# Optimization experiments

Measured on AMD Instinct MI355X. Metric: run time of the kernel, lower is better.

Reference implementation:

```python
import jax, jax.numpy as jnp
import numpy as np

D_IN = 1024
D_OUT = 1024
CTX_LEN = 2048
BATCH = 4
SEQ = 2048


def setup_inputs() -> dict:
    key = jax.random.key(0)
    kx, kq, kk, kv = jax.random.split(key, 4)
    x = jax.random.normal(kx, (BATCH, SEQ, D_IN), dtype=jnp.float32)
    s = 1.0 / np.sqrt(D_IN)
    # torch nn.Linear weight is (d_out, d_in); store transposed for x @ W
    W_q = jax.random.uniform(kq, (D_IN, D_OUT), dtype=jnp.float32, minval=-s, maxval=s)
    W_k = jax.random.uniform(kk, (D_IN, D_OUT), dtype=jnp.float32, minval=-s, maxval=s)
    W_v = jax.random.uniform(kv, (D_IN, D_OUT), dtype=jnp.float32, minval=-s, maxval=s)
    return {"x": x, "W_q": W_q, "W_k": W_k, "W_v": W_v}


def reference(x, W_q, W_k, W_v):
    b, n, _ = x.shape
    d_out = W_q.shape[1]
    q = x @ W_q            # [b, n, d_out]
    k = x @ W_k
    v = x @ W_v
    scores = jnp.einsum('bqd,bkd->bqk', q, k)  # [b, n, n]
    causal = jnp.triu(jnp.ones((n, n), dtype=bool), k=1)
    scores = jnp.where(causal, -jnp.inf, scores)
    attn = jax.nn.softmax(scores / jnp.sqrt(jnp.float32(d_out)), axis=-1)
    # dropout p=0.0 -> identity
    return jnp.einsum('bqk,bkd->bqd', attn, v)
```

## Files before the change

kernel.cpp:

```cpp
#include <hip/hip_runtime.h>
#include <hip/hip_bf16.h>

#define BATCH 4
#define SEQ   2048
#define DIN   1024
#define DOUT  1024
#define N3    3072
#define MTOT  (BATCH*SEQ)

typedef __hip_bfloat16 bf16;
typedef __attribute__((ext_vector_type(8))) short bf16x8;
typedef __attribute__((ext_vector_type(4))) float f32x4;

#define MFMA(a,b,c) __builtin_amdgcn_mfma_f32_16x16x32_bf16(a,b,c,0,0,0)

union pack4 { bf16 h[4]; uint2 u2; };
union pack8 { bf16 h[8]; bf16x8 v; };

__device__ __forceinline__ void gl16(const bf16* g, bf16* l)
{
    __builtin_amdgcn_global_load_lds(
        (const __attribute__((address_space(1))) void*)g,
        (__attribute__((address_space(3))) void*)l, 16, 0, 0);
}


__global__ __launch_bounds__(256)
void k_cvt_x(const float* __restrict__ x, bf16* __restrict__ xb)
{
    long i = ((long)blockIdx.x * 256 + threadIdx.x) * 4;
    float4 v = *(const float4*)(x + i);
    pack4 o;
    o.h[0] = __float2bfloat16(v.x);
    o.h[1] = __float2bfloat16(v.y);
    o.h[2] = __float2bfloat16(v.z);
    o.h[3] = __float2bfloat16(v.w);
    *(uint2*)(xb + i) = o.u2;
}

__global__ __launch_bounds__(256)
void k_cvt_w(const float* __restrict__ Wq, const float* __restrict__ Wk,
             const float* __restrict__ Wv, bf16* __restrict__ Wt)
{
    __shared__ bf16 t[64][68];
    const int mat = blockIdx.z;
    const float* W = (mat == 0) ? Wq : ((mat == 1) ? Wk : Wv);
    const int k0 = blockIdx.y * 64, n0 = blockIdx.x * 64;
#pragma unroll
    for (int p = 0; p < 4; ++p) {
        int kr = p * 16 + (threadIdx.x >> 4);
        int c4 = (threadIdx.x & 15) * 4;
        float4 v = *(const float4*)&W[(long)(k0 + kr) * DOUT + n0 + c4];
        t[c4 + 0][kr] = __float2bfloat16(v.x);
        t[c4 + 1][kr] = __float2bfloat16(v.y);
        t[c4 + 2][kr] = __float2bfloat16(v.z);
        t[c4 + 3][kr] = __float2bfloat16(v.w);
    }
    __syncthreads();
    bf16* O = Wt + (long)mat * DIN * DOUT;
#pragma unroll
    for (int i = 0; i < 2; ++i) {
        int l = threadIdx.x + i * 256;
        int n = l >> 3, c8 = (l & 7) * 8;
        pack8 o;
#pragma unroll
        for (int j = 0; j < 8; ++j) o.h[j] = t[n][c8 + j];
        *(bf16x8*)&O[(long)(n0 + n) * DIN + k0 + c8] = o.v;
    }
}


__device__ __forceinline__ void gemm_core(
    const bf16* __restrict__ Ab, long lda,
    const bf16* __restrict__ Bb, long ldb,
    int nk, bf16* __restrict__ As, bf16* __restrict__ Bs,
    f32x4 acc[4][4])
{
    const int tid  = threadIdx.x;
    const int lane = tid & 63;
    const int wave = tid >> 6;
    const int wm = (wave >> 1) * 64;
    const int wn = (wave & 1) * 64;
    const int r  = lane & 15;
    const int qd = lane >> 4;

    const int row0 = tid >> 3;
    const int c    = (tid & 7) ^ (row0 & 7);
    const long aoff = (long)row0 * lda + c * 8;
    const long boff = (long)row0 * ldb + c * 8;
    const long astep = 32 * lda, bstep = 32 * ldb;
    bf16* dA = &As[tid * 8];
    bf16* dB = &Bs[tid * 8];

    for (int kk = 0; kk < nk; ++kk) {
        const bf16* A = Ab + kk * 64 + aoff;
        const bf16* B = Bb + kk * 64 + boff;
#pragma unroll
        for (int i = 0; i < 4; ++i) {
            gl16(A + i * astep, dA + i * 2048);
            gl16(B + i * bstep, dB + i * 2048);
        }
        __syncthreads();
#pragma unroll
        for (int ks = 0; ks < 2; ++ks) {
            const int slot = ((ks * 4 + qd) ^ (r & 7)) * 8;
            bf16x8 af[4], bv[4];
#pragma unroll
            for (int mi = 0; mi < 4; ++mi)
                af[mi] = *(const bf16x8*)&As[(wm + mi * 16 + r) * 64 + slot];
#pragma unroll
            for (int ni = 0; ni < 4; ++ni)
                bv[ni] = *(const bf16x8*)&Bs[(wn + ni * 16 + r) * 64 + slot];
#pragma unroll
            for (int mi = 0; mi < 4; ++mi)
#pragma unroll
                for (int ni = 0; ni < 4; ++ni)
                    acc[mi][ni] = MFMA(af[mi], bv[ni], acc[mi][ni]);
        }
        __syncthreads();
    }
}


__global__ __launch_bounds__(256)
void k_gemm_qkv(const bf16* __restrict__ xb, const bf16* __restrict__ Wt,
                bf16* __restrict__ QKV)
{
    __shared__ __align__(16) bf16 As[128 * 64];
    __shared__ __align__(16) bf16 Bs[128 * 64];
    const int m0 = blockIdx.y * 128, n0 = blockIdx.x * 128;
    f32x4 acc[4][4] = {};
    gemm_core(xb + (long)m0 * DIN, DIN, Wt + (long)n0 * DIN, DIN, DIN / 64, As, Bs, acc);

    const int lane = threadIdx.x & 63, wave = threadIdx.x >> 6;
    const int wm = (wave >> 1) * 64, wn = (wave & 1) * 64;
    const int r = lane & 15, qd = lane >> 4;
#pragma unroll
    for (int mi = 0; mi < 4; ++mi)
#pragma unroll
        for (int ni = 0; ni < 4; ++ni)
#pragma unroll
            for (int j = 0; j < 4; ++j) {
                int row = m0 + wm + mi * 16 + qd * 4 + j;
                int col = n0 + wn + ni * 16 + r;
                QKV[(long)row * N3 + col] = __float2bfloat16(acc[mi][ni][j]);
            }
}


__global__ __launch_bounds__(256)
void k_transpose_v(const bf16* __restrict__ QKV, bf16* __restrict__ Vt)
{
    __shared__ __align__(16) bf16 t[64][80];
    const int b = blockIdx.z;
    const int s0 = blockIdx.x * 64, d0 = blockIdx.y * 64;
    const bf16* Vb = QKV + (long)b * SEQ * N3 + 2048;
#pragma unroll
    for (int i = 0; i < 2; ++i) {
        int l = threadIdx.x + i * 256;
        int sl = l >> 3, c8 = (l & 7) * 8;
        *(bf16x8*)&t[sl][c8] = *(const bf16x8*)&Vb[(long)(s0 + sl) * N3 + d0 + c8];
    }
    __syncthreads();
    bf16* Ob = Vt + (long)b * DOUT * SEQ;
#pragma unroll
    for (int i = 0; i < 2; ++i) {
        int l = threadIdx.x + i * 256;
        int dl = l >> 3, s8 = (l & 7) * 8;
        pack8 o;
#pragma unroll
        for (int j = 0; j < 8; ++j) o.h[j] = t[s8 + j][dl];
        *(bf16x8*)&Ob[(long)(d0 + dl) * SEQ + s0 + s8] = o.v;
    }
}


__global__ __launch_bounds__(256)
void k_gemm_scores(const bf16* __restrict__ QKV, bf16* __restrict__ P,
                   float* __restrict__ rowSum)
{
    const int b = blockIdx.z, qt = blockIdx.y, kt = blockIdx.x;
    if (kt > qt) return;
    __shared__ __align__(16) bf16 As[128 * 64];
    __shared__ __align__(16) bf16 Bs[128 * 64];
    const bf16* A  = QKV + (long)b * SEQ * N3;
    const bf16* Bt = A + 1024;
    f32x4 acc[4][4] = {};
    gemm_core(A + (long)qt * 128 * N3, N3, Bt + (long)kt * 128 * N3, N3,
              DIN / 64, As, Bs, acc);

    bf16* Pb = P + (long)b * SEQ * SEQ;
    float* RS = rowSum + b * SEQ;
    const int lane = threadIdx.x & 63, wave = threadIdx.x >> 6;
    const int wm = (wave >> 1) * 64, wn = (wave & 1) * 64;
    const int r = lane & 15, qd = lane >> 4;

    float rp[4][4];
#pragma unroll
    for (int mi = 0; mi < 4; ++mi)
#pragma unroll
        for (int j = 0; j < 4; ++j) rp[mi][j] = 0.f;

#pragma unroll
    for (int mi = 0; mi < 4; ++mi)
#pragma unroll
        for (int ni = 0; ni < 4; ++ni)
#pragma unroll
            for (int j = 0; j < 4; ++j) {
                int row = qt * 128 + wm + mi * 16 + qd * 4 + j;
                int col = kt * 128 + wn + ni * 16 + r;
                float e = (col > row) ? 0.f : __expf(acc[mi][ni][j] * 0.03125f);
                rp[mi][j] += e;
                Pb[(long)row * SEQ + col] = __float2bfloat16(e);
            }
#pragma unroll
    for (int d = 1; d < 16; d <<= 1)
#pragma unroll
        for (int mi = 0; mi < 4; ++mi)
#pragma unroll
            for (int j = 0; j < 4; ++j)
                rp[mi][j] += __shfl_xor(rp[mi][j], d, 64);
    if (r == 0) {
#pragma unroll
        for (int mi = 0; mi < 4; ++mi)
#pragma unroll
            for (int j = 0; j < 4; ++j) {
                int row = qt * 128 + wm + mi * 16 + qd * 4 + j;
                atomicAdd(&RS[row], rp[mi][j]);
            }
    }
}


__global__ __launch_bounds__(256)
void k_gemm_pv(const bf16* __restrict__ P, const bf16* __restrict__ Vt,
               const float* __restrict__ rowSum, float* __restrict__ O)
{
    const int b = blockIdx.z, nt = blockIdx.x;
    const int qt = (SEQ / 128 - 1) - blockIdx.y;
    __shared__ __align__(16) bf16 As[128 * 64];
    __shared__ __align__(16) bf16 Bs[128 * 64];
    const bf16* A  = P + (long)b * SEQ * SEQ + (long)qt * 128 * SEQ;
    const bf16* Bt = Vt + (long)b * DOUT * SEQ;
    const int nk = (qt + 1) * 2;
    f32x4 acc[4][4] = {};
    gemm_core(A, SEQ, Bt + (long)nt * 128 * SEQ, SEQ, nk, As, Bs, acc);

    float* Ob = O + (long)b * SEQ * DOUT;
    const float* RS = rowSum + b * SEQ;
    const int lane = threadIdx.x & 63, wave = threadIdx.x >> 6;
    const int wm = (wave >> 1) * 64, wn = (wave & 1) * 64;
    const int r = lane & 15, qd = lane >> 4;
#pragma unroll
    for (int mi = 0; mi < 4; ++mi)
#pragma unroll
        for (int j = 0; j < 4; ++j) {
            int row = qt * 128 + wm + mi * 16 + qd * 4 + j;
            float inv = 1.0f / RS[row];
#pragma unroll
            for (int ni = 0; ni < 4; ++ni) {
                int col = nt * 128 + wn + ni * 16 + r;
                Ob[(long)row * DOUT + col] = acc[mi][ni][j] * inv;
            }
        }
}


extern "C" void kernel_launch(void* const* d_in, const int* in_sizes, int n_in,
                              void* d_out, int out_size, void* d_ws, size_t ws_size,
                              hipStream_t stream)
{
    const float* x  = (const float*)d_in[0];
    const float* Wq = (const float*)d_in[1];
    const float* Wk = (const float*)d_in[2];
    const float* Wv = (const float*)d_in[3];
    float* out = (float*)d_out;

    char* ws = (char*)d_ws;
    bf16*  xb  = (bf16*)(ws);
    bf16*  Wt  = (bf16*)(ws + 16777216);
    bf16*  QKV = (bf16*)(ws + 23068672);
    bf16*  Vt  = (bf16*)(ws + 73400320);
    bf16*  P   = (bf16*)(ws + 90177536);
    float* RS  = (float*)(ws + 123731968);

    hipMemsetAsync(RS, 0, BATCH * SEQ * sizeof(float), stream);
    k_cvt_x<<<dim3(MTOT * DIN / (256 * 4)), 256, 0, stream>>>(x, xb);
    k_cvt_w<<<dim3(DOUT / 64, DIN / 64, 3), 256, 0, stream>>>(Wq, Wk, Wv, Wt);
    k_gemm_qkv<<<dim3(N3 / 128, MTOT / 128), 256, 0, stream>>>(xb, Wt, QKV);
    k_transpose_v<<<dim3(SEQ / 64, DOUT / 64, BATCH), 256, 0, stream>>>(QKV, Vt);
    k_gemm_scores<<<dim3(SEQ / 128, SEQ / 128, BATCH), 256, 0, stream>>>(QKV, P, RS);
    k_gemm_pv<<<dim3(DOUT / 128, SEQ / 128, BATCH), 256, 0, stream>>>(P, Vt, RS, out);
}
```

Before: 254.1 us.

## Fuse V transpose into QKV GEMM epilogue and merge conversion kernels

The QKV projection epilogue now writes Q/K into a compact 2048-wide buffer and transposes V tiles through shared memory directly into Vt, which removes the separate transpose kernel and its extra read and write of V. The x and weight conversion kernels are merged into one launch, and the scores and PV kernels get a launch-bounds occupancy hint of three blocks. This saves two launches and a round trip of V through memory. In exchange the V epilogue adds shared-memory staging and a barrier, and the occupancy hint may push the compiler to spill registers.

```diff
diff --git a/kernel.cpp b/kernel.cpp
--- a/kernel.cpp
+++ b/kernel.cpp
@@ -26,26 +26,28 @@
 
 
 __global__ __launch_bounds__(256)
-void k_cvt_x(const float* __restrict__ x, bf16* __restrict__ xb)
-{
-    long i = ((long)blockIdx.x * 256 + threadIdx.x) * 4;
-    float4 v = *(const float4*)(x + i);
-    pack4 o;
-    o.h[0] = __float2bfloat16(v.x);
-    o.h[1] = __float2bfloat16(v.y);
-    o.h[2] = __float2bfloat16(v.z);
-    o.h[3] = __float2bfloat16(v.w);
-    *(uint2*)(xb + i) = o.u2;
-}
-
-__global__ __launch_bounds__(256)
-void k_cvt_w(const float* __restrict__ Wq, const float* __restrict__ Wk,
-             const float* __restrict__ Wv, bf16* __restrict__ Wt)
+void k_prep(const float* __restrict__ x, const float* __restrict__ Wq,
+            const float* __restrict__ Wk, const float* __restrict__ Wv,
+            bf16* __restrict__ xb, bf16* __restrict__ Wt)
 {
     __shared__ bf16 t[64][68];
-    const int mat = blockIdx.z;
+    const int bid = blockIdx.x;
+    if (bid < 8192) {
+        long i = ((long)bid * 256 + threadIdx.x) * 4;
+        float4 v = *(const float4*)(x + i);
+        pack4 o;
+        o.h[0] = __float2bfloat16(v.x);
+        o.h[1] = __float2bfloat16(v.y);
+        o.h[2] = __float2bfloat16(v.z);
+        o.h[3] = __float2bfloat16(v.w);
+        *(uint2*)(xb + i) = o.u2;
+        return;
+    }
+    const int idx = bid - 8192;
+    const int mat = idx >> 8;
+    const int rem = idx & 255;
+    const int k0 = (rem >> 4) * 64, n0 = (rem & 15) * 64;
     const float* W = (mat == 0) ? Wq : ((mat == 1) ? Wk : Wv);
-    const int k0 = blockIdx.y * 64, n0 = blockIdx.x * 64;
 #pragma unroll
     for (int p = 0; p < 4; ++p) {
         int kr = p * 16 + (threadIdx.x >> 4);
@@ -124,69 +126,73 @@
 
 __global__ __launch_bounds__(256)
 void k_gemm_qkv(const bf16* __restrict__ xb, const bf16* __restrict__ Wt,
-                bf16* __restrict__ QKV)
-{
-    __shared__ __align__(16) bf16 As[128 * 64];
-    __shared__ __align__(16) bf16 Bs[128 * 64];
+                bf16* __restrict__ QK, bf16* __restrict__ Vt)
+{
+    __shared__ __align__(16) bf16 smem[17408];
+    bf16* As = smem;
+    bf16* Bs = smem + 8192;
     const int m0 = blockIdx.y * 128, n0 = blockIdx.x * 128;
     f32x4 acc[4][4] = {};
     gemm_core(xb + (long)m0 * DIN, DIN, Wt + (long)n0 * DIN, DIN, DIN / 64, As, Bs, acc);
 
-    const int lane = threadIdx.x & 63, wave = threadIdx.x >> 6;
+    const int tid = threadIdx.x;
+    const int lane = tid & 63, wave = tid >> 6;
     const int wm = (wave >> 1) * 64, wn = (wave & 1) * 64;
     const int r = lane & 15, qd = lane >> 4;
-#pragma unroll
-    for (int mi = 0; mi < 4; ++mi)
-#pragma unroll
-        for (int ni = 0; ni < 4; ++ni)
-#pragma unroll
-            for (int j = 0; j < 4; ++j) {
-                int row = m0 + wm + mi * 16 + qd * 4 + j;
-                int col = n0 + wn + ni * 16 + r;
-                QKV[(long)row * N3 + col] = __float2bfloat16(acc[mi][ni][j]);
-            }
-}
-
-
-__global__ __launch_bounds__(256)
-void k_transpose_v(const bf16* __restrict__ QKV, bf16* __restrict__ Vt)
-{
-    __shared__ __align__(16) bf16 t[64][80];
-    const int b = blockIdx.z;
-    const int s0 = blockIdx.x * 64, d0 = blockIdx.y * 64;
-    const bf16* Vb = QKV + (long)b * SEQ * N3 + 2048;
-#pragma unroll
-    for (int i = 0; i < 2; ++i) {
-        int l = threadIdx.x + i * 256;
-        int sl = l >> 3, c8 = (l & 7) * 8;
-        *(bf16x8*)&t[sl][c8] = *(const bf16x8*)&Vb[(long)(s0 + sl) * N3 + d0 + c8];
-    }
-    __syncthreads();
-    bf16* Ob = Vt + (long)b * DOUT * SEQ;
-#pragma unroll
-    for (int i = 0; i < 2; ++i) {
-        int l = threadIdx.x + i * 256;
-        int dl = l >> 3, s8 = (l & 7) * 8;
-        pack8 o;
-#pragma unroll
-        for (int j = 0; j < 8; ++j) o.h[j] = t[s8 + j][dl];
-        *(bf16x8*)&Ob[(long)(d0 + dl) * SEQ + s0 + s8] = o.v;
-    }
-}
-
-
-__global__ __launch_bounds__(256)
-void k_gemm_scores(const bf16* __restrict__ QKV, bf16* __restrict__ P,
+
+    if (n0 < 2048) {
+#pragma unroll
+        for (int mi = 0; mi < 4; ++mi)
+#pragma unroll
+            for (int ni = 0; ni < 4; ++ni)
+#pragma unroll
+                for (int j = 0; j < 4; ++j) {
+                    int row = m0 + wm + mi * 16 + qd * 4 + j;
+                    int col = n0 + wn + ni * 16 + r;
+                    QK[(long)row * 2048 + col] = __float2bfloat16(acc[mi][ni][j]);
+                }
+    } else {
+        const int ld = 136;
+        bf16* T = smem;
+#pragma unroll
+        for (int mi = 0; mi < 4; ++mi)
+#pragma unroll
+            for (int ni = 0; ni < 4; ++ni) {
+                pack4 p;
+#pragma unroll
+                for (int j = 0; j < 4; ++j) p.h[j] = __float2bfloat16(acc[mi][ni][j]);
+                int d_l = wn + ni * 16 + r;
+                int s_l = wm + mi * 16 + qd * 4;
+                *(uint2*)&T[d_l * ld + s_l] = p.u2;
+            }
+        __syncthreads();
+        const int n0v = n0 - 2048;
+        const int bb = m0 >> 11;
+        const int s0 = m0 & 2047;
+        bf16* Ob = Vt + (long)bb * DOUT * SEQ + s0;
+#pragma unroll
+        for (int p = 0; p < 8; ++p) {
+            int l = tid + p * 256;
+            int d = l >> 4, s8 = (l & 15) * 8;
+            bf16x8 vv = *(const bf16x8*)&T[d * ld + s8];
+            *(bf16x8*)&Ob[(long)(n0v + d) * SEQ + s8] = vv;
+        }
+    }
+}
+
+
+__global__ __launch_bounds__(256, 3)
+void k_gemm_scores(const bf16* __restrict__ QK, bf16* __restrict__ P,
                    float* __restrict__ rowSum)
 {
     const int b = blockIdx.z, qt = blockIdx.y, kt = blockIdx.x;
     if (kt > qt) return;
     __shared__ __align__(16) bf16 As[128 * 64];
     __shared__ __align__(16) bf16 Bs[128 * 64];
-    const bf16* A  = QKV + (long)b * SEQ * N3;
+    const bf16* A  = QK + (long)b * SEQ * 2048;
     const bf16* Bt = A + 1024;
     f32x4 acc[4][4] = {};
-    gemm_core(A + (long)qt * 128 * N3, N3, Bt + (long)kt * 128 * N3, N3,
+    gemm_core(A + (long)qt * 128 * 2048, 2048, Bt + (long)kt * 128 * 2048, 2048,
               DIN / 64, As, Bs, acc);
 
     bf16* Pb = P + (long)b * SEQ * SEQ;
@@ -232,7 +238,7 @@
 }
 
 
-__global__ __launch_bounds__(256)
+__global__ __launch_bounds__(256, 3)
 void k_gemm_pv(const bf16* __restrict__ P, const bf16* __restrict__ Vt,
                const float* __restrict__ rowSum, float* __restrict__ O)
 {
@@ -277,18 +283,16 @@
     float* out = (float*)d_out;
 
     char* ws = (char*)d_ws;
-    bf16*  xb  = (bf16*)(ws);
-    bf16*  Wt  = (bf16*)(ws + 16777216);
-    bf16*  QKV = (bf16*)(ws + 23068672);
-    bf16*  Vt  = (bf16*)(ws + 73400320);
-    bf16*  P   = (bf16*)(ws + 90177536);
-    float* RS  = (float*)(ws + 123731968);
+    bf16*  xb = (bf16*)(ws);
+    bf16*  Wt = (bf16*)(ws + 16777216);
+    bf16*  QK = (bf16*)(ws + 23068672);
+    bf16*  Vt = (bf16*)(ws + 56623104);
+    bf16*  P  = (bf16*)(ws + 73400320);
+    float* RS = (float*)(ws + 106954752);
 
     hipMemsetAsync(RS, 0, BATCH * SEQ * sizeof(float), stream);
-    k_cvt_x<<<dim3(MTOT * DIN / (256 * 4)), 256, 0, stream>>>(x, xb);
-    k_cvt_w<<<dim3(DOUT / 64, DIN / 64, 3), 256, 0, stream>>>(Wq, Wk, Wv, Wt);
-    k_gemm_qkv<<<dim3(N3 / 128, MTOT / 128), 256, 0, stream>>>(xb, Wt, QKV);
-    k_transpose_v<<<dim3(SEQ / 64, DOUT / 64, BATCH), 256, 0, stream>>>(QKV, Vt);
-    k_gemm_scores<<<dim3(SEQ / 128, SEQ / 128, BATCH), 256, 0, stream>>>(QKV, P, RS);
+    k_prep<<<dim3(8192 + 768), 256, 0, stream>>>(x, Wq, Wk, Wv, xb, Wt);
+    k_gemm_qkv<<<dim3(N3 / 128, MTOT / 128), 256, 0, stream>>>(xb, Wt, QK, Vt);
+    k_gemm_scores<<<dim3(SEQ / 128, SEQ / 128, BATCH), 256, 0, stream>>>(QK, P, RS);
     k_gemm_pv<<<dim3(DOUT / 128, SEQ / 128, BATCH), 256, 0, stream>>>(P, Vt, RS, out);
 }
```

New measurement: 225.1 us. -11.4%, faster.
